# Optimization experiments

Measured on AMD Instinct MI355X. Metric: run time of the kernel, lower is better.

The kernel has to match this reference:

```python
import jax, jax.numpy as jnp
import numpy as np

SIZE = 1024
HEADS = 16
HEAD_SIZE = SIZE // HEADS
B, S = 2, 2048


def setup_inputs() -> dict:
    key = jax.random.key(0)
    ks = jax.random.split(key, 12)
    def lin(kw, kb, fan_in, fan_out):
        # mimic nn.Linear default init U(-1/sqrt(fan_in), 1/sqrt(fan_in))
        bound = 1.0 / np.sqrt(fan_in)
        W = jax.random.uniform(kw, (fan_out, fan_in), jnp.float32, -bound, bound)
        b = jax.random.uniform(kb, (fan_out,), jnp.float32, -bound, bound)
        return W, b
    Wk, bk = lin(ks[0], ks[1], SIZE, SIZE)
    Wv, bv = lin(ks[2], ks[3], SIZE, SIZE)
    Wq, bq = lin(ks[4], ks[5], SIZE, SIZE)
    Wo, bo = lin(ks[6], ks[7], SIZE, SIZE)
    k_in = jax.random.normal(ks[8], (B, S, SIZE), jnp.float32)
    v_in = jax.random.normal(ks[9], (B, S, SIZE), jnp.float32)
    q_in = jax.random.normal(ks[10], (B, S, SIZE), jnp.float32)
    # causal mask: True = masked out (as in torch masked_fill_)
    mask = jnp.triu(jnp.ones((S, S), dtype=bool), k=1)
    return {"key": k_in, "value": v_in, "query": q_in, "mask": mask,
            "Wk": Wk, "bk": bk, "Wv": Wv, "bv": bv,
            "Wq": Wq, "bq": bq, "Wo": Wo, "bo": bo}


def _shape(x):
    # [B, S, size] -> [B, H, S, head_size]
    b, s, _ = x.shape
    return x.reshape(b, s, HEADS, HEAD_SIZE).transpose(0, 2, 1, 3)


def reference(key, value, query, mask, Wk, bk, Wv, bv, Wq, bq, Wo, bo):
    k = _shape(key @ Wk.T + bk)      # [B,H,S,D]
    v = _shape(value @ Wv.T + bv)
    q = _shape(query @ Wq.T + bq)
    scale = jnp.sqrt(jnp.float32(HEAD_SIZE))
    scores = jnp.einsum('bhqd,bhkd->bhqk', q, k) / scale
    scores = jnp.where(mask, -jnp.inf, scores)
    attn = jax.nn.softmax(scores, axis=-1)
    out = jnp.einsum('bhqk,bhkd->bhqd', attn, v)  # [B,H,S,D]
    out = out.transpose(0, 2, 1, 3).reshape(out.shape[0], out.shape[2], SIZE)
    out = out @ Wo.T + bo
    return out, attn
```

## Files before the change

kernel.cpp:

```cpp
#include <hip/hip_runtime.h>
#include <stdint.h>

typedef unsigned short u16_t;
typedef unsigned int   u32_t;
using short8 = __attribute__((ext_vector_type(8))) short;
using f32x4  = __attribute__((ext_vector_type(4))) float;

#define SEQ   2048
#define SZ    1024
#define NH    16
#define DH    64
#define NBH   32
#define MTOK  4096

#define GPTR(p) ((__attribute__((address_space(1))) void*)(uintptr_t)(p))
#define LPTR(p) ((__attribute__((address_space(3))) void*)(p))

__device__ __forceinline__ u16_t f2bf(float f) {
  union { float f; u32_t i; } v; v.f = f;
  return (u16_t)((v.i + 0x7FFFu + ((v.i >> 16) & 1u)) >> 16);
}

union pk8 { u16_t u[8]; uint4 v; };
__device__ __forceinline__ uint4 cvt8(const float* src) {
  pk8 p;
  #pragma unroll
  for (int i = 0; i < 8; i++) p.u[i] = f2bf(src[i]);
  return p.v;
}

struct CvtArgs { const float* s[7]; u16_t* d[7]; int n[7]; };

__global__ __launch_bounds__(256) void cvt_bf16(CvtArgs a) {
  const int seg = blockIdx.y;
  const float* __restrict__ src = a.s[seg];
  u16_t* __restrict__ dst = a.d[seg];
  const int n8 = a.n[seg] >> 3;
  for (int i = blockIdx.x * 256 + threadIdx.x; i < n8; i += gridDim.x * 256) {
    float f[8];
    *(float4*)&f[0] = ((const float4*)src)[(size_t)i * 2];
    *(float4*)&f[4] = ((const float4*)src)[(size_t)i * 2 + 1];
    ((uint4*)dst)[i] = cvt8(f);
  }
}

template<int OUTF32, int VTW>
__global__ __launch_bounds__(256) void gemm_bt(
    const u16_t* __restrict__ A, const u16_t* __restrict__ W,
    const float* __restrict__ bias, void* __restrict__ Cv,
    const int M, const int N, const int K)
{
  __shared__ __align__(16) u16_t sA[128 * 32];
  __shared__ __align__(16) u16_t sB[64 * 32];
  const int t = threadIdx.x;
  const int w = t >> 6, lane = t & 63, q = lane >> 4, l16 = lane & 15;
  const int wm = (w >> 1) * 64, wn = (w & 1) * 32;
  const int m0 = blockIdx.y * 128, n0 = blockIdx.x * 64;
  const int r0 = t >> 2;
  const int c0 = (t & 3) * 8;
  const u16_t* Ap = &A[(size_t)(m0 + r0) * K + c0];
  const u16_t* Bp = &W[(size_t)(n0 + r0) * K + c0];

  f32x4 acc[4][2] = {};

  for (int kb = 0; kb < K; kb += 32) {
    __builtin_amdgcn_global_load_lds(GPTR(Ap + kb),                  LPTR(&sA[t * 8]),        16, 0, 0);
    __builtin_amdgcn_global_load_lds(GPTR(Ap + (size_t)64 * K + kb), LPTR(&sA[2048 + t * 8]), 16, 0, 0);
    __builtin_amdgcn_global_load_lds(GPTR(Bp + kb),                  LPTR(&sB[t * 8]),        16, 0, 0);
    __syncthreads();
    short8 af[4], bf[2];
    #pragma unroll
    for (int i = 0; i < 4; i++)
      af[i] = *(const short8*)&sA[(wm + i * 16 + l16) * 32 + q * 8];
    #pragma unroll
    for (int j = 0; j < 2; j++)
      bf[j] = *(const short8*)&sB[(wn + j * 16 + l16) * 32 + q * 8];
    #pragma unroll
    for (int mi = 0; mi < 4; mi++)
      #pragma unroll
      for (int ni = 0; ni < 2; ni++)
        acc[mi][ni] = __builtin_amdgcn_mfma_f32_16x16x32_bf16(af[mi], bf[ni], acc[mi][ni], 0, 0, 0);
    __syncthreads();
  }

  #pragma unroll
  for (int ni = 0; ni < 2; ni++) {
    const int cg = n0 + wn + ni * 16 + l16;
    const float bv = bias[cg];
    #pragma unroll
    for (int mi = 0; mi < 4; mi++) {
      const int rg0 = m0 + wm + mi * 16 + q * 4;
      if (OUTF32) {
        float* C = (float*)Cv;
        #pragma unroll
        for (int r = 0; r < 4; r++)
          C[(size_t)(rg0 + r) * N + cg] = acc[mi][ni][r] + bv;
      } else if (VTW == 0) {
        u16_t* C = (u16_t*)Cv;
        #pragma unroll
        for (int r = 0; r < 4; r++)
          C[(size_t)(rg0 + r) * N + cg] = f2bf(acc[mi][ni][r] + bv);
      } else {
        u16_t* C = (u16_t*)Cv;
        const int trow = ((rg0 >> 11) * NH + (cg >> 6)) * DH + (cg & (DH - 1));
        const int s0 = rg0 & (SEQ - 1);
        union { u16_t u[4]; uint2 v; } pk;
        #pragma unroll
        for (int r = 0; r < 4; r++) pk.u[r] = f2bf(acc[mi][ni][r] + bv);
        *(uint2*)&C[(size_t)trow * SEQ + s0] = pk.v;
      }
    }
  }
}

__global__ __launch_bounds__(256) void attn_fused(
    const u16_t* __restrict__ Qp, const u16_t* __restrict__ Kp,
    const u16_t* __restrict__ VT, float* __restrict__ attn,
    u16_t* __restrict__ AO)
{
  __shared__ __align__(16) u16_t Pbuf[4][16 * 32];
  const int t = threadIdx.x;
  const int w = t >> 6, lane = t & 63, q = lane >> 4, l16 = lane & 15;
  const int bh = blockIdx.x, b = bh >> 4;
  const int h = bh & (NH - 1);
  float* attn_bh = attn + (size_t)bh * SEQ * SEQ;

  #pragma unroll 1
  for (int hh = 0; hh < 2; hh++) {
    const int y = hh ? (31 - (int)blockIdx.y) : (int)blockIdx.y;
    const int i0 = y * 64;
    const int wrow0 = i0 + w * 16;
    const size_t qbase = ((size_t)(b * SEQ + wrow0 + l16)) * SZ + h * DH + q * 8;
    const short8 qf0 = *(const short8*)&Qp[qbase];
    const short8 qf1 = *(const short8*)&Qp[qbase + 32];
    const int tmax = (i0 >> 4) + w;
    const int njt  = (i0 >> 4) + 4;

    float l[4] = {0.f, 0.f, 0.f, 0.f};
    for (int jt = 0; jt <= tmax; jt++) {
      const int j0 = jt * 16;
      const size_t kbase = ((size_t)(b * SEQ + j0 + l16)) * SZ + h * DH + q * 8;
      const short8 kf0 = *(const short8*)&Kp[kbase];
      const short8 kf1 = *(const short8*)&Kp[kbase + 32];
      f32x4 s = {};
      s = __builtin_amdgcn_mfma_f32_16x16x32_bf16(qf0, kf0, s, 0, 0, 0);
      s = __builtin_amdgcn_mfma_f32_16x16x32_bf16(qf1, kf1, s, 0, 0, 0);
      #pragma unroll
      for (int r = 0; r < 4; r++) {
        const int row = wrow0 + q * 4 + r;
        const int col = j0 + l16;
        l[r] += (col <= row) ? __expf(s[r] * 0.125f) : 0.0f;
      }
    }
    float rl[4];
    #pragma unroll
    for (int r = 0; r < 4; r++) {
      float ps = l[r];
      ps += __shfl_xor(ps, 1);
      ps += __shfl_xor(ps, 2);
      ps += __shfl_xor(ps, 4);
      ps += __shfl_xor(ps, 8);
      rl[r] = 1.0f / ps;
    }

    {
      const int zc0 = (y + 1) * 64;
      const int nz4 = (SEQ - zc0) >> 2;
      const uint4 z = make_uint4(0u, 0u, 0u, 0u);
      for (int r = 0; r < 16; r++) {
        uint4* d4 = (uint4*)(attn_bh + (size_t)(wrow0 + r) * SEQ + zc0);
        for (int c = lane; c < nz4; c += 64) d4[c] = z;
      }
    }

    f32x4 o[4] = {};
    for (int pr = 0; pr < njt / 2; pr++) {
      const int t0 = pr * 2;
      if (t0 > tmax) {
        #pragma unroll
        for (int uu = 0; uu < 2; uu++) {
          const int j0 = (t0 + uu) * 16;
          #pragma unroll
          for (int r = 0; r < 4; r++)
            attn_bh[(size_t)(wrow0 + q * 4 + r) * SEQ + j0 + l16] = 0.0f;
        }
        continue;
      }
      #pragma unroll
      for (int uu = 0; uu < 2; uu++) {
        const int jt = t0 + uu, j0 = jt * 16;
        const size_t kbase = ((size_t)(b * SEQ + j0 + l16)) * SZ + h * DH + q * 8;
        const short8 kf0 = *(const short8*)&Kp[kbase];
        const short8 kf1 = *(const short8*)&Kp[kbase + 32];
        f32x4 s = {};
        s = __builtin_amdgcn_mfma_f32_16x16x32_bf16(qf0, kf0, s, 0, 0, 0);
        s = __builtin_amdgcn_mfma_f32_16x16x32_bf16(qf1, kf1, s, 0, 0, 0);
        #pragma unroll
        for (int r = 0; r < 4; r++) {
          const int row = wrow0 + q * 4 + r;
          const int col = j0 + l16;
          const float p = (col <= row) ? __expf(s[r] * 0.125f) * rl[r] : 0.0f;
          attn_bh[(size_t)row * SEQ + col] = p;
          Pbuf[w][(q * 4 + r) * 32 + uu * 16 + l16] = f2bf(p);
        }
      }
      __asm__ volatile("s_waitcnt lgkmcnt(0)" ::: "memory");
      const short8 pf = *(const short8*)&Pbuf[w][l16 * 32 + q * 8];
      #pragma unroll
      for (int n = 0; n < 4; n++) {
        const size_t vbase = ((size_t)(bh * DH + n * 16 + l16)) * SEQ + t0 * 16 + q * 8;
        const short8 vf = *(const short8*)&VT[vbase];
        o[n] = __builtin_amdgcn_mfma_f32_16x16x32_bf16(pf, vf, o[n], 0, 0, 0);
      }
    }

    #pragma unroll
    for (int n = 0; n < 4; n++)
      #pragma unroll
      for (int r = 0; r < 4; r++)
        AO[(size_t)(b * SEQ + wrow0 + q * 4 + r) * SZ + h * DH + n * 16 + l16] = f2bf(o[n][r]);
  }
}

extern "C" void kernel_launch(void* const* d_in, const int* in_sizes, int n_in,
                              void* d_out, int out_size, void* d_ws, size_t ws_size,
                              hipStream_t stream) {
  const float* key   = (const float*)d_in[0];
  const float* value = (const float*)d_in[1];
  const float* query = (const float*)d_in[2];
  const float* Wk = (const float*)d_in[4];
  const float* bk = (const float*)d_in[5];
  const float* Wv = (const float*)d_in[6];
  const float* bv = (const float*)d_in[7];
  const float* Wq = (const float*)d_in[8];
  const float* bq = (const float*)d_in[9];
  const float* Wo = (const float*)d_in[10];
  const float* bo = (const float*)d_in[11];

  float* out  = (float*)d_out;
  float* attn = out + (size_t)MTOK * SZ;

  u16_t* Qp  = (u16_t*)d_ws;
  u16_t* Kp  = Qp  + (size_t)MTOK * SZ;
  u16_t* VTv = Kp  + (size_t)MTOK * SZ;
  u16_t* AO  = VTv + (size_t)MTOK * SZ;
  u16_t* Qb  = AO  + (size_t)MTOK * SZ;
  u16_t* Kb  = Qb  + (size_t)MTOK * SZ;
  u16_t* Vb  = Kb  + (size_t)MTOK * SZ;
  u16_t* Wqb = Vb  + (size_t)MTOK * SZ;
  u16_t* Wkb = Wqb + (size_t)SZ * SZ;
  u16_t* Wvb = Wkb + (size_t)SZ * SZ;
  u16_t* Wob = Wvb + (size_t)SZ * SZ;

  CvtArgs ca;
  ca.s[0] = query; ca.d[0] = Qb;  ca.n[0] = MTOK * SZ;
  ca.s[1] = key;   ca.d[1] = Kb;  ca.n[1] = MTOK * SZ;
  ca.s[2] = value; ca.d[2] = Vb;  ca.n[2] = MTOK * SZ;
  ca.s[3] = Wq;    ca.d[3] = Wqb; ca.n[3] = SZ * SZ;
  ca.s[4] = Wk;    ca.d[4] = Wkb; ca.n[4] = SZ * SZ;
  ca.s[5] = Wv;    ca.d[5] = Wvb; ca.n[5] = SZ * SZ;
  ca.s[6] = Wo;    ca.d[6] = Wob; ca.n[6] = SZ * SZ;
  cvt_bf16<<<dim3(256, 7), 256, 0, stream>>>(ca);

  const dim3 gg(SZ / 64, MTOK / 128);
  gemm_bt<0, 0><<<gg, 256, 0, stream>>>(Qb, Wqb, bq, Qp,  MTOK, SZ, SZ);
  gemm_bt<0, 0><<<gg, 256, 0, stream>>>(Kb, Wkb, bk, Kp,  MTOK, SZ, SZ);
  gemm_bt<0, 1><<<gg, 256, 0, stream>>>(Vb, Wvb, bv, VTv, MTOK, SZ, SZ);
  attn_fused<<<dim3(NBH, 16), 256, 0, stream>>>(Qp, Kp, VTv, attn, AO);
  gemm_bt<1, 0><<<gg, 256, 0, stream>>>(AO, Wob, bo, out, MTOK, SZ, SZ);
}
```

Measured before the change: 853.8 us.

## Batch QKV GEMMs into one launch, split attention blocks, use nontemporal attn stores

The three Q/K/V projection GEMMs now run as one launch using blockIdx.z, with larger 128x128 tiles for more data reuse. The attention kernel drops the two-row-block loop per block in favour of a 32-deep grid, reverses block order so the longest rows start first, and adds a 4-blocks-per-CU occupancy hint. All stores to the large fp32 attention matrix, including the zero fill, become nontemporal to reduce cache pollution. Trade-offs: the larger tiles raise register pressure, and dropping the paired short/long rows may leave the causal workload less balanced across blocks.

```diff
diff --git a/kernel.cpp b/kernel.cpp
--- a/kernel.cpp
+++ b/kernel.cpp
@@ -5,6 +5,7 @@
 typedef unsigned int   u32_t;
 using short8 = __attribute__((ext_vector_type(8))) short;
 using f32x4  = __attribute__((ext_vector_type(4))) float;
+using u32x4  = __attribute__((ext_vector_type(4))) unsigned int;
 
 #define SEQ   2048
 #define SZ    1024
@@ -44,10 +45,77 @@
   }
 }
 
-template<int OUTF32, int VTW>
+struct QkvArgs {
+  const u16_t* A[3]; const u16_t* W[3]; const float* bias[3]; u16_t* out[3];
+};
+
+__global__ __launch_bounds__(256) void gemm_qkv(QkvArgs ga)
+{
+  __shared__ __align__(16) u16_t sA[128 * 32];
+  __shared__ __align__(16) u16_t sB[128 * 32];
+  const int z = blockIdx.z;
+  const u16_t* __restrict__ A    = ga.A[z];
+  const u16_t* __restrict__ W    = ga.W[z];
+  const float* __restrict__ bias = ga.bias[z];
+  u16_t* __restrict__ C          = ga.out[z];
+  const int K = SZ;
+  const int t = threadIdx.x;
+  const int w = t >> 6, lane = t & 63, q = lane >> 4, l16 = lane & 15;
+  const int wm = (w >> 1) * 64, wn = (w & 1) * 64;
+  const int m0 = blockIdx.y * 128, n0 = blockIdx.x * 128;
+  const int r0 = t >> 2;
+  const int c0 = (t & 3) * 8;
+  const u16_t* Ap = &A[(size_t)(m0 + r0) * K + c0];
+  const u16_t* Bp = &W[(size_t)(n0 + r0) * K + c0];
+
+  f32x4 acc[4][4] = {};
+
+  for (int kb = 0; kb < K; kb += 32) {
+    __builtin_amdgcn_global_load_lds(GPTR(Ap + kb),                  LPTR(&sA[t * 8]),        16, 0, 0);
+    __builtin_amdgcn_global_load_lds(GPTR(Ap + (size_t)64 * K + kb), LPTR(&sA[2048 + t * 8]), 16, 0, 0);
+    __builtin_amdgcn_global_load_lds(GPTR(Bp + kb),                  LPTR(&sB[t * 8]),        16, 0, 0);
+    __builtin_amdgcn_global_load_lds(GPTR(Bp + (size_t)64 * K + kb), LPTR(&sB[2048 + t * 8]), 16, 0, 0);
+    __syncthreads();
+    short8 af[4], bf[4];
+    #pragma unroll
+    for (int i = 0; i < 4; i++) {
+      af[i] = *(const short8*)&sA[(wm + i * 16 + l16) * 32 + q * 8];
+      bf[i] = *(const short8*)&sB[(wn + i * 16 + l16) * 32 + q * 8];
+    }
+    #pragma unroll
+    for (int mi = 0; mi < 4; mi++)
+      #pragma unroll
+      for (int ni = 0; ni < 4; ni++)
+        acc[mi][ni] = __builtin_amdgcn_mfma_f32_16x16x32_bf16(af[mi], bf[ni], acc[mi][ni], 0, 0, 0);
+    __syncthreads();
+  }
+
+  #pragma unroll
+  for (int ni = 0; ni < 4; ni++) {
+    const int cg = n0 + wn + ni * 16 + l16;
+    const float bv = bias[cg];
+    #pragma unroll
+    for (int mi = 0; mi < 4; mi++) {
+      const int rg0 = m0 + wm + mi * 16 + q * 4;
+      if (z < 2) {
+        #pragma unroll
+        for (int r = 0; r < 4; r++)
+          C[(size_t)(rg0 + r) * SZ + cg] = f2bf(acc[mi][ni][r] + bv);
+      } else {
+        const int trow = ((rg0 >> 11) * NH + (cg >> 6)) * DH + (cg & (DH - 1));
+        const int s0 = rg0 & (SEQ - 1);
+        union { u16_t u[4]; uint2 v; } pk;
+        #pragma unroll
+        for (int r = 0; r < 4; r++) pk.u[r] = f2bf(acc[mi][ni][r] + bv);
+        *(uint2*)&C[(size_t)trow * SEQ + s0] = pk.v;
+      }
+    }
+  }
+}
+
 __global__ __launch_bounds__(256) void gemm_bt(
     const u16_t* __restrict__ A, const u16_t* __restrict__ W,
-    const float* __restrict__ bias, void* __restrict__ Cv,
+    const float* __restrict__ bias, float* __restrict__ C,
     const int M, const int N, const int K)
 {
   __shared__ __align__(16) u16_t sA[128 * 32];
@@ -90,30 +158,14 @@
     #pragma unroll
     for (int mi = 0; mi < 4; mi++) {
       const int rg0 = m0 + wm + mi * 16 + q * 4;
-      if (OUTF32) {
-        float* C = (float*)Cv;
-        #pragma unroll
-        for (int r = 0; r < 4; r++)
-          C[(size_t)(rg0 + r) * N + cg] = acc[mi][ni][r] + bv;
-      } else if (VTW == 0) {
-        u16_t* C = (u16_t*)Cv;
-        #pragma unroll
-        for (int r = 0; r < 4; r++)
-          C[(size_t)(rg0 + r) * N + cg] = f2bf(acc[mi][ni][r] + bv);
-      } else {
-        u16_t* C = (u16_t*)Cv;
-        const int trow = ((rg0 >> 11) * NH + (cg >> 6)) * DH + (cg & (DH - 1));
-        const int s0 = rg0 & (SEQ - 1);
-        union { u16_t u[4]; uint2 v; } pk;
-        #pragma unroll
-        for (int r = 0; r < 4; r++) pk.u[r] = f2bf(acc[mi][ni][r] + bv);
-        *(uint2*)&C[(size_t)trow * SEQ + s0] = pk.v;
-      }
-    }
-  }
-}
-
-__global__ __launch_bounds__(256) void attn_fused(
+      #pragma unroll
+      for (int r = 0; r < 4; r++)
+        C[(size_t)(rg0 + r) * N + cg] = acc[mi][ni][r] + bv;
+    }
+  }
+}
+
+__global__ __launch_bounds__(256, 4) void attn_fused(
     const u16_t* __restrict__ Qp, const u16_t* __restrict__ Kp,
     const u16_t* __restrict__ VT, float* __restrict__ attn,
     u16_t* __restrict__ AO)
@@ -125,20 +177,71 @@
   const int h = bh & (NH - 1);
   float* attn_bh = attn + (size_t)bh * SEQ * SEQ;
 
-  #pragma unroll 1
-  for (int hh = 0; hh < 2; hh++) {
-    const int y = hh ? (31 - (int)blockIdx.y) : (int)blockIdx.y;
-    const int i0 = y * 64;
-    const int wrow0 = i0 + w * 16;
-    const size_t qbase = ((size_t)(b * SEQ + wrow0 + l16)) * SZ + h * DH + q * 8;
-    const short8 qf0 = *(const short8*)&Qp[qbase];
-    const short8 qf1 = *(const short8*)&Qp[qbase + 32];
-    const int tmax = (i0 >> 4) + w;
-    const int njt  = (i0 >> 4) + 4;
-
-    float l[4] = {0.f, 0.f, 0.f, 0.f};
-    for (int jt = 0; jt <= tmax; jt++) {
-      const int j0 = jt * 16;
+  const int y = 31 - (int)blockIdx.y;
+  const int i0 = y * 64;
+  const int wrow0 = i0 + w * 16;
+  const size_t qbase = ((size_t)(b * SEQ + wrow0 + l16)) * SZ + h * DH + q * 8;
+  const short8 qf0 = *(const short8*)&Qp[qbase];
+  const short8 qf1 = *(const short8*)&Qp[qbase + 32];
+  const int tmax = (i0 >> 4) + w;
+  const int njt  = (i0 >> 4) + 4;
+
+  float l[4] = {0.f, 0.f, 0.f, 0.f};
+  #pragma unroll 2
+  for (int jt = 0; jt <= tmax; jt++) {
+    const int j0 = jt * 16;
+    const size_t kbase = ((size_t)(b * SEQ + j0 + l16)) * SZ + h * DH + q * 8;
+    const short8 kf0 = *(const short8*)&Kp[kbase];
+    const short8 kf1 = *(const short8*)&Kp[kbase + 32];
+    f32x4 s = {};
+    s = __builtin_amdgcn_mfma_f32_16x16x32_bf16(qf0, kf0, s, 0, 0, 0);
+    s = __builtin_amdgcn_mfma_f32_16x16x32_bf16(qf1, kf1, s, 0, 0, 0);
+    #pragma unroll
+    for (int r = 0; r < 4; r++) {
+      const int row = wrow0 + q * 4 + r;
+      const int col = j0 + l16;
+      l[r] += (col <= row) ? __expf(s[r] * 0.125f) : 0.0f;
+    }
+  }
+  float rl[4];
+  #pragma unroll
+  for (int r = 0; r < 4; r++) {
+    float ps = l[r];
+    ps += __shfl_xor(ps, 1);
+    ps += __shfl_xor(ps, 2);
+    ps += __shfl_xor(ps, 4);
+    ps += __shfl_xor(ps, 8);
+    rl[r] = 1.0f / ps;
+  }
+
+  {
+    const int zc0 = (y + 1) * 64;
+    const int nz4 = (SEQ - zc0) >> 2;
+    const u32x4 z = {0u, 0u, 0u, 0u};
+    for (int r = 0; r < 16; r++) {
+      u32x4* d4 = (u32x4*)(attn_bh + (size_t)(wrow0 + r) * SEQ + zc0);
+      for (int c = lane; c < nz4; c += 64)
+        __builtin_nontemporal_store(z, d4 + c);
+    }
+  }
+
+  f32x4 o[4] = {};
+  for (int pr = 0; pr < njt / 2; pr++) {
+    const int t0 = pr * 2;
+    if (t0 > tmax) {
+      #pragma unroll
+      for (int uu = 0; uu < 2; uu++) {
+        const int j0 = (t0 + uu) * 16;
+        #pragma unroll
+        for (int r = 0; r < 4; r++)
+          __builtin_nontemporal_store(
+              0.0f, &attn_bh[(size_t)(wrow0 + q * 4 + r) * SEQ + j0 + l16]);
+      }
+      continue;
+    }
+    #pragma unroll
+    for (int uu = 0; uu < 2; uu++) {
+      const int jt = t0 + uu, j0 = jt * 16;
       const size_t kbase = ((size_t)(b * SEQ + j0 + l16)) * SZ + h * DH + q * 8;
       const short8 kf0 = *(const short8*)&Kp[kbase];
       const short8 kf1 = *(const short8*)&Kp[kbase + 32];
@@ -149,77 +252,26 @@
       for (int r = 0; r < 4; r++) {
         const int row = wrow0 + q * 4 + r;
         const int col = j0 + l16;
-        l[r] += (col <= row) ? __expf(s[r] * 0.125f) : 0.0f;
+        const float p = (col <= row) ? __expf(s[r] * 0.125f) * rl[r] : 0.0f;
+        __builtin_nontemporal_store(p, &attn_bh[(size_t)row * SEQ + col]);
+        Pbuf[w][(q * 4 + r) * 32 + uu * 16 + l16] = f2bf(p);
       }
     }
-    float rl[4];
-    #pragma unroll
-    for (int r = 0; r < 4; r++) {
-      float ps = l[r];
-      ps += __shfl_xor(ps, 1);
-      ps += __shfl_xor(ps, 2);
-      ps += __shfl_xor(ps, 4);
-      ps += __shfl_xor(ps, 8);
-      rl[r] = 1.0f / ps;
-    }
-
-    {
-      const int zc0 = (y + 1) * 64;
-      const int nz4 = (SEQ - zc0) >> 2;
-      const uint4 z = make_uint4(0u, 0u, 0u, 0u);
-      for (int r = 0; r < 16; r++) {
-        uint4* d4 = (uint4*)(attn_bh + (size_t)(wrow0 + r) * SEQ + zc0);
-        for (int c = lane; c < nz4; c += 64) d4[c] = z;
-      }
-    }
-
-    f32x4 o[4] = {};
-    for (int pr = 0; pr < njt / 2; pr++) {
-      const int t0 = pr * 2;
-      if (t0 > tmax) {
-        #pragma unroll
-        for (int uu = 0; uu < 2; uu++) {
-          const int j0 = (t0 + uu) * 16;
-          #pragma unroll
-          for (int r = 0; r < 4; r++)
-            attn_bh[(size_t)(wrow0 + q * 4 + r) * SEQ + j0 + l16] = 0.0f;
-        }
-        continue;
-      }
-      #pragma unroll
-      for (int uu = 0; uu < 2; uu++) {
-        const int jt = t0 + uu, j0 = jt * 16;
-        const size_t kbase = ((size_t)(b * SEQ + j0 + l16)) * SZ + h * DH + q * 8;
-        const short8 kf0 = *(const short8*)&Kp[kbase];
-        const short8 kf1 = *(const short8*)&Kp[kbase + 32];
-        f32x4 s = {};
-        s = __builtin_amdgcn_mfma_f32_16x16x32_bf16(qf0, kf0, s, 0, 0, 0);
-        s = __builtin_amdgcn_mfma_f32_16x16x32_bf16(qf1, kf1, s, 0, 0, 0);
-        #pragma unroll
-        for (int r = 0; r < 4; r++) {
-          const int row = wrow0 + q * 4 + r;
-          const int col = j0 + l16;
-          const float p = (col <= row) ? __expf(s[r] * 0.125f) * rl[r] : 0.0f;
-          attn_bh[(size_t)row * SEQ + col] = p;
-          Pbuf[w][(q * 4 + r) * 32 + uu * 16 + l16] = f2bf(p);
-        }
-      }
-      __asm__ volatile("s_waitcnt lgkmcnt(0)" ::: "memory");
-      const short8 pf = *(const short8*)&Pbuf[w][l16 * 32 + q * 8];
-      #pragma unroll
-      for (int n = 0; n < 4; n++) {
-        const size_t vbase = ((size_t)(bh * DH + n * 16 + l16)) * SEQ + t0 * 16 + q * 8;
-        const short8 vf = *(const short8*)&VT[vbase];
-        o[n] = __builtin_amdgcn_mfma_f32_16x16x32_bf16(pf, vf, o[n], 0, 0, 0);
-      }
-    }
-
-    #pragma unroll
-    for (int n = 0; n < 4; n++)
-      #pragma unroll
-      for (int r = 0; r < 4; r++)
-        AO[(size_t)(b * SEQ + wrow0 + q * 4 + r) * SZ + h * DH + n * 16 + l16] = f2bf(o[n][r]);
-  }
+    __asm__ volatile("s_waitcnt lgkmcnt(0)" ::: "memory");
+    const short8 pf = *(const short8*)&Pbuf[w][l16 * 32 + q * 8];
+    #pragma unroll
+    for (int n = 0; n < 4; n++) {
+      const size_t vbase = ((size_t)(bh * DH + n * 16 + l16)) * SEQ + t0 * 16 + q * 8;
+      const short8 vf = *(const short8*)&VT[vbase];
+      o[n] = __builtin_amdgcn_mfma_f32_16x16x32_bf16(pf, vf, o[n], 0, 0, 0);
+    }
+  }
+
+  #pragma unroll
+  for (int n = 0; n < 4; n++)
+    #pragma unroll
+    for (int r = 0; r < 4; r++)
+      AO[(size_t)(b * SEQ + wrow0 + q * 4 + r) * SZ + h * DH + n * 16 + l16] = f2bf(o[n][r]);
 }
 
 extern "C" void kernel_launch(void* const* d_in, const int* in_sizes, int n_in,
@@ -262,10 +314,13 @@
   ca.s[6] = Wo;    ca.d[6] = Wob; ca.n[6] = SZ * SZ;
   cvt_bf16<<<dim3(256, 7), 256, 0, stream>>>(ca);
 
-  const dim3 gg(SZ / 64, MTOK / 128);
-  gemm_bt<0, 0><<<gg, 256, 0, stream>>>(Qb, Wqb, bq, Qp,  MTOK, SZ, SZ);
-  gemm_bt<0, 0><<<gg, 256, 0, stream>>>(Kb, Wkb, bk, Kp,  MTOK, SZ, SZ);
-  gemm_bt<0, 1><<<gg, 256, 0, stream>>>(Vb, Wvb, bv, VTv, MTOK, SZ, SZ);
-  attn_fused<<<dim3(NBH, 16), 256, 0, stream>>>(Qp, Kp, VTv, attn, AO);
-  gemm_bt<1, 0><<<gg, 256, 0, stream>>>(AO, Wob, bo, out, MTOK, SZ, SZ);
-}
+  QkvArgs ga;
+  ga.A[0] = Qb;  ga.W[0] = Wqb; ga.bias[0] = bq; ga.out[0] = Qp;
+  ga.A[1] = Kb;  ga.W[1] = Wkb; ga.bias[1] = bk; ga.out[1] = Kp;
+  ga.A[2] = Vb;  ga.W[2] = Wvb; ga.bias[2] = bv; ga.out[2] = VTv;
+  gemm_qkv<<<dim3(SZ / 128, MTOK / 128, 3), 256, 0, stream>>>(ga);
+
+  attn_fused<<<dim3(NBH, 32), 256, 0, stream>>>(Qp, Kp, VTv, attn, AO);
+
+  gemm_bt<<<dim3(SZ / 64, MTOK / 128), 256, 0, stream>>>(AO, Wob, bo, out, MTOK, SZ, SZ);
+}
```

Measured after the change: 817.7 us. 1.04x faster.
